# Performance work log

Measured on AMD Instinct MI355X. Metric: run time of the kernel, lower is better.

## Reference

```python
import jax, jax.numpy as jnp
import numpy as np

BETA = 0.25
GAMMA = 0.9
EPS = 1e-05
B, H, W, D, K = 64, 32, 32, 256, 1024


def setup_inputs() -> dict:
    key = jax.random.key(0)
    k1, k2 = jax.random.split(key)
    return {
        "inputs": jax.random.normal(k1, (B, H, W, D), dtype=jnp.float32),
        "codebook": jax.random.normal(k2, (D, K), dtype=jnp.float32),
        "ema_hidden_cluster": jnp.zeros((K,), dtype=jnp.float32),
        "ema_hidden_dw": jnp.zeros((D, K), dtype=jnp.float32),
        "counter": 1,  # counter after increment (fresh state: 0 + 1)
    }


def reference(inputs, codebook, ema_hidden_cluster, ema_hidden_dw, counter):
    d, k = codebook.shape
    flat = inputs.reshape(-1, d)  # [N, D]
    distances = (
        jnp.sum(jnp.square(flat), 1, keepdims=True)
        - 2.0 * jnp.matmul(flat, codebook)
        + jnp.sum(jnp.square(codebook), 0, keepdims=True)
    )
    encoding_indices = jnp.argmin(distances, axis=1)  # [N]
    encodings = jax.nn.one_hot(encoding_indices, k, dtype=distances.dtype)  # [N, K]
    flat_quantized = jnp.take(codebook, encoding_indices, axis=1).swapaxes(1, 0)  # [N, D]
    quantized = flat_quantized.reshape(inputs.shape)
    loss = BETA * jnp.mean(jnp.square(jax.lax.stop_gradient(quantized) - inputs))

    # --- EMA codebook update (training=True path) ---
    decay = jnp.float32(GAMMA)
    one = jnp.float32(1.0)
    bias = one - jnp.power(decay, counter)
    cluster_size = jnp.sum(encodings, axis=0)  # [K]
    hid_cs = ema_hidden_cluster * decay + cluster_size * (one - decay)
    avg_cs = hid_cs / bias
    dw = jnp.matmul(flat.T, encodings)  # [D, K]
    hid_dw = ema_hidden_dw * decay + dw * (one - decay)
    avg_dw = hid_dw / bias
    n = jnp.sum(avg_cs)
    smoothed_cs = (avg_cs + EPS) / (n + k * EPS) * n
    new_codebook = avg_dw / smoothed_cs[None, :]

    ste = inputs + jax.lax.stop_gradient(quantized - inputs)
    avg_probs = jnp.mean(encodings, 0)
    perplexity = jnp.exp(-jnp.sum(avg_probs * jnp.log(avg_probs + 1e-10)))
    return (ste, perplexity, loss, new_codebook)
```

## Files before the change

### kernel.cpp

```cpp
#include <hip/hip_runtime.h>

#define N 65536
#define D 256
#define K 1024
#define BETA 0.25f
#define GAMMA 0.9f
#define EPS 1e-5f

#define DWROWS 64

#define OFF_INDICES 0
#define OFF_PERM    262144
#define OFF_COUNTS  524288
#define OFF_CNORM   528384
#define OFF_OFFSETS 532480
#define OFF_CURSOR  536576
#define OFF_SMOOTH  540672
#define OFF_LOSSP   544768
#define OFF_CBT     546816
#define OFF_CBE     1595392

typedef __bf16 bf16x8 __attribute__((ext_vector_type(8)));
typedef short  s16x8  __attribute__((ext_vector_type(8)));
typedef float  f32x4  __attribute__((ext_vector_type(4)));

__device__ inline unsigned short f32_to_bf16_rn(float f) {
    unsigned int u = __float_as_uint(f);
    unsigned int r = u + 0x7fffu + ((u >> 16) & 1u);
    return (unsigned short)(r >> 16);
}

__device__ inline f32x4 mfma16(s16x8 a, s16x8 b, f32x4 c) {
    return __builtin_amdgcn_mfma_f32_16x16x32_bf16(
        __builtin_bit_cast(bf16x8, a), __builtin_bit_cast(bf16x8, b), c, 0, 0, 0);
}

__device__ __forceinline__ void stage16(const s16x8* __restrict__ g, s16x8* l) {
    __builtin_amdgcn_global_load_lds(
        (const __attribute__((address_space(1))) void*)g,
        (__attribute__((address_space(3))) void*)l, 16, 0, 0);
}

__global__ __launch_bounds__(256) void pack_cb(const float* __restrict__ cb,
                                               float* __restrict__ cbT,
                                               s16x8* __restrict__ cbEp,
                                               float* __restrict__ cnorm) {
    const int ct = blockIdx.x >> 3;
    const int c2 = (blockIdx.x >> 1) & 3;
    const int half = blockIdx.x & 1;
    const int u = half * 256 + threadIdx.x;
    const int frgc = u >> 7;
    const int ks = (u >> 6) & 1;
    const int L = u & 63;
    const int c = ct * 64 + frgc * 16 + (L & 15);
    const int d0 = c2 * 64 + (ks * 4 + (L >> 4)) * 8;
    float v[8];
    s16x8 hv, lv;
    float ss = 0.f;
#pragma unroll
    for (int j = 0; j < 8; ++j) {
        float f = cb[(size_t)(d0 + j) * K + c];
        v[j] = f;
        unsigned short h = f32_to_bf16_rn(f);
        hv[j] = (short)h;
        lv[j] = (short)f32_to_bf16_rn(f - __uint_as_float((unsigned)h << 16));
        ss = fmaf(f, f, ss);
    }
    *(float4*)&cbT[(size_t)c * D + d0]     = make_float4(v[0], v[1], v[2], v[3]);
    *(float4*)&cbT[(size_t)c * D + d0 + 4] = make_float4(v[4], v[5], v[6], v[7]);
    cbEp[(size_t)(ct * 8 + c2) * 512 + u]     = hv;
    cbEp[(size_t)(ct * 8 + 4 + c2) * 512 + u] = lv;
    atomicAdd(&cnorm[c], ss);
}

__global__ __launch_bounds__(256, 2) void argmin_mfma_kernel(
        const float* __restrict__ x,
        const s16x8* __restrict__ cbEp,
        const float* __restrict__ cnorm,
        int* __restrict__ indices) {
    __shared__ s16x8 Bs[2][1024];

    const int tid = threadIdx.x;
    const int lane = tid & 63;
    const int w = tid >> 6;
    const int r0 = blockIdx.x * 128;
    const int row16 = lane & 15;
    const int quad = lane >> 4;

#pragma unroll
    for (int i = 0; i < 4; ++i)
        stage16(cbEp + i * 256 + tid, &Bs[0][i * 256 + w * 64]);

    s16x8 Ah[2][8], Al[2][8];
#pragma unroll
    for (int frg = 0; frg < 2; ++frg) {
#pragma unroll
        for (int kb8 = 0; kb8 < 8; ++kb8) {
            const float* src = &x[(size_t)(r0 + w * 32 + frg * 16 + row16) * D
                                  + kb8 * 32 + quad * 8];
            float4 v0 = *(const float4*)src;
            float4 v1 = *(const float4*)(src + 4);
            float f[8] = {v0.x, v0.y, v0.z, v0.w, v1.x, v1.y, v1.z, v1.w};
            s16x8 hv, lv;
#pragma unroll
            for (int j = 0; j < 8; ++j) {
                unsigned short h = f32_to_bf16_rn(f[j]);
                hv[j] = (short)h;
                lv[j] = (short)f32_to_bf16_rn(f[j] - __uint_as_float((unsigned)h << 16));
            }
            Ah[frg][kb8] = hv;
            Al[frg][kb8] = lv;
        }
    }

    float minv[2][4];
    int   mini[2][4];
#pragma unroll
    for (int frg = 0; frg < 2; ++frg)
#pragma unroll
        for (int reg = 0; reg < 4; ++reg) { minv[frg][reg] = 3.4e38f; mini[frg][reg] = 0; }

    for (int ct = 0; ct < 16; ++ct) {
        f32x4 acc[2][4];
#pragma unroll
        for (int frg = 0; frg < 2; ++frg)
#pragma unroll
            for (int fc = 0; fc < 4; ++fc) acc[frg][fc] = (f32x4){0.f, 0.f, 0.f, 0.f};

#pragma unroll
        for (int ph = 0; ph < 4; ++ph) {
            __syncthreads();
            const bool has_next = !(ct == 15 && ph == 3);
            if (has_next) {
                const int nct = (ph == 3) ? ct + 1 : ct;
                const int nph = (ph == 3) ? 0 : ph + 1;
                const size_t gb = (size_t)(nct * 8 + nph * 2) * 512;
#pragma unroll
                for (int i = 0; i < 4; ++i)
                    stage16(cbEp + gb + i * 256 + tid, &Bs[(ph + 1) & 1][i * 256 + w * 64]);
            }
#pragma unroll
            for (int half = 0; half < 2; ++half) {
                const int cchunk = ph * 2 + half;
                const int c2 = cchunk & 3;
#pragma unroll
                for (int ks = 0; ks < 2; ++ks) {
                    const int ksb = c2 * 2 + ks;
#pragma unroll
                    for (int fc = 0; fc < 4; ++fc) {
                        s16x8 b = Bs[ph & 1][half * 512 + (fc * 2 + ks) * 64 + lane];
#pragma unroll
                        for (int frg = 0; frg < 2; ++frg) {
                            acc[frg][fc] = mfma16(Ah[frg][ksb], b, acc[frg][fc]);
                            if (cchunk < 4)
                                acc[frg][fc] = mfma16(Al[frg][ksb], b, acc[frg][fc]);
                        }
                    }
                }
            }
        }
#pragma unroll
        for (int fc = 0; fc < 4; ++fc) {
            int col = ct * 64 + fc * 16 + row16;
            float cn = cnorm[col];
#pragma unroll
            for (int frg = 0; frg < 2; ++frg)
#pragma unroll
                for (int reg = 0; reg < 4; ++reg) {
                    float val = fmaf(-2.f, acc[frg][fc][reg], cn);
                    if (val < minv[frg][reg]) { minv[frg][reg] = val; mini[frg][reg] = col; }
                }
        }
    }

#pragma unroll
    for (int mask = 1; mask <= 8; mask <<= 1) {
#pragma unroll
        for (int frg = 0; frg < 2; ++frg)
#pragma unroll
            for (int reg = 0; reg < 4; ++reg) {
                float ov = __shfl_xor(minv[frg][reg], mask, 64);
                int   oi = __shfl_xor(mini[frg][reg], mask, 64);
                if (ov < minv[frg][reg] ||
                    (ov == minv[frg][reg] && oi < mini[frg][reg])) {
                    minv[frg][reg] = ov; mini[frg][reg] = oi;
                }
            }
    }
    if (row16 == 0) {
#pragma unroll
        for (int frg = 0; frg < 2; ++frg)
#pragma unroll
            for (int reg = 0; reg < 4; ++reg)
                indices[r0 + w * 32 + frg * 16 + quad * 4 + reg] = mini[frg][reg];
    }
}

__global__ __launch_bounds__(1024) void finalize_kernel(const int* __restrict__ indices,
                                                        const float* __restrict__ ema_c,
                                                        const int* __restrict__ counter,
                                                        float* __restrict__ out_perp,
                                                        int* __restrict__ cursor,
                                                        float* __restrict__ smoothed) {
    const int k = threadIdx.x;
    const int lane = k & 63;
    const int wave = k >> 6;
    __shared__ int hist[1024];
    __shared__ float wsum[16], went[16];
    __shared__ int wtot[16];

    hist[k] = 0;
    __syncthreads();
    const int4* idx4 = (const int4*)indices;
#pragma unroll 4
    for (int i = 0; i < 16; ++i) {
        int4 v = idx4[(size_t)i * 1024 + k];
        atomicAdd(&hist[v.x], 1);
        atomicAdd(&hist[v.y], 1);
        atomicAdd(&hist[v.z], 1);
        atomicAdd(&hist[v.w], 1);
    }
    __syncthreads();

    const int c = hist[k];
    const float bias = 1.0f - powf(GAMMA, (float)counter[0]);
    const float avg = fmaf(ema_c[k], GAMMA, (float)c * (1.0f - GAMMA)) / bias;
    const float p = (float)c * (1.0f / (float)N);
    const float ent = p * logf(p + 1e-10f);

    float a = avg, e = ent;
#pragma unroll
    for (int off = 32; off >= 1; off >>= 1) {
        a += __shfl_down(a, off, 64);
        e += __shfl_down(e, off, 64);
    }
    int v = c;
#pragma unroll
    for (int off = 1; off < 64; off <<= 1) {
        int t = __shfl_up(v, off, 64);
        if (lane >= off) v += t;
    }
    if (lane == 0)  { wsum[wave] = a; went[wave] = e; }
    if (lane == 63) { wtot[wave] = v; }
    __syncthreads();

    float nsum = 0.f, entt = 0.f;
    int woff = 0;
#pragma unroll
    for (int i = 0; i < 16; ++i) {
        nsum += wsum[i];
        entt += went[i];
        if (i < wave) woff += wtot[i];
    }
    cursor[k] = woff + v - c;
    smoothed[k] = (avg + EPS) / (nsum + (float)K * EPS) * nsum;
    if (k == 0) out_perp[0] = expf(-entt);
}

__global__ __launch_bounds__(256) void scatter_kernel(const int* __restrict__ indices,
                                                      int* __restrict__ cursor,
                                                      int* __restrict__ permk,
                                                      float* __restrict__ dwT) {
    const int n = blockIdx.x * 256 + threadIdx.x;
    *(float4*)&dwT[(size_t)n * 4] = make_float4(0.f, 0.f, 0.f, 0.f);
    const int k = indices[n];
    const int pos = atomicAdd(&cursor[k], 1);
    permk[pos] = n | (k << 16);
}

__global__ __launch_bounds__(256) void dw_fused_kernel(const float* __restrict__ x,
                                                       const float* __restrict__ cbT,
                                                       const int* __restrict__ permk,
                                                       float* __restrict__ ste,
                                                       float* __restrict__ dwT,
                                                       float* __restrict__ lossp) {
    __shared__ int s_rows[DWROWS];
    __shared__ int s_keys[DWROWS];
    const int tid = threadIdx.x;
    const int g = tid >> 6;
    const int d4 = tid & 63;
    const int base = blockIdx.x * DWROWS;
    if (tid < DWROWS) {
        const int pk = permk[base + tid];
        s_rows[tid] = pk & 0xffff;
        s_keys[tid] = pk >> 16;
    }
    __syncthreads();

    const float4* x4   = (const float4*)x;
    const float4* cbT4 = (const float4*)cbT;
    float4*       ste4 = (float4*)ste;

    float ax = 0.f, ay = 0.f, az = 0.f, aw = 0.f;
    float ls = 0.f;
    const int r0 = g * 16;
#pragma unroll
    for (int i = 0; i < 16; ++i) {
        const int r = r0 + i;
        const int n = s_rows[r];
        const int k = s_keys[r];
        const float4 xv = x4[(size_t)n * 64 + d4];
        const float4 q  = cbT4[(size_t)k * 64 + d4];
        ste4[(size_t)n * 64 + d4] = q;
        ax += xv.x; ay += xv.y; az += xv.z; aw += xv.w;
        float dx = q.x - xv.x, dy = q.y - xv.y, dz = q.z - xv.z, dw = q.w - xv.w;
        ls = fmaf(dx, dx, ls); ls = fmaf(dy, dy, ls);
        ls = fmaf(dz, dz, ls); ls = fmaf(dw, dw, ls);
        const int nk = (i == 15) ? -1 : s_keys[r + 1];
        if (nk != k) {
            float* dst = &dwT[(size_t)k * D + d4 * 4];
            atomicAdd(dst + 0, ax);
            atomicAdd(dst + 1, ay);
            atomicAdd(dst + 2, az);
            atomicAdd(dst + 3, aw);
            ax = ay = az = aw = 0.f;
        }
    }
#pragma unroll
    for (int off = 32; off >= 1; off >>= 1) ls += __shfl_down(ls, off, 64);
    __shared__ float red[4];
    if ((tid & 63) == 0) red[tid >> 6] = ls;
    __syncthreads();
    if (tid == 0) lossp[blockIdx.x] = red[0] + red[1] + red[2] + red[3];
}

__global__ __launch_bounds__(256) void codebook_final_kernel(const float* __restrict__ dwT,
                                                             const float* __restrict__ ema_dw,
                                                             const float* __restrict__ smoothed,
                                                             const int* __restrict__ counter,
                                                             const float* __restrict__ lossp,
                                                             float* __restrict__ out_cb,
                                                             float* __restrict__ out_loss) {
    __shared__ float tile[64][65];
    __shared__ float lred[4];
    const int tid = threadIdx.x;

    if (blockIdx.x == 0) {
        float s = lossp[tid] + lossp[tid + 256] + lossp[tid + 512] + lossp[tid + 768];
#pragma unroll
        for (int off = 32; off >= 1; off >>= 1) s += __shfl_down(s, off, 64);
        if ((tid & 63) == 0) lred[tid >> 6] = s;
        __syncthreads();
        if (tid == 0)
            out_loss[0] = BETA * (lred[0] + lred[1] + lred[2] + lred[3])
                          * (1.0f / ((float)N * (float)D));
        __syncthreads();
    }

    const int d0 = (blockIdx.x & 3) * 64;
    const int k0 = (blockIdx.x >> 2) * 64;
#pragma unroll
    for (int it = 0; it < 16; ++it) {
        int idx = it * 256 + tid;
        int kk = idx >> 6, dd = idx & 63;
        tile[kk][dd] = dwT[(size_t)(k0 + kk) * D + d0 + dd];
    }
    __syncthreads();
    const float bias = 1.0f - powf(GAMMA, (float)counter[0]);
#pragma unroll
    for (int it = 0; it < 16; ++it) {
        int idx = it * 256 + tid;
        int dd = idx >> 6, kk = idx & 63;
        float dwv = tile[kk][dd];
        float hid = fmaf(ema_dw[(size_t)(d0 + dd) * K + k0 + kk], GAMMA,
                         dwv * (1.0f - GAMMA));
        out_cb[(size_t)(d0 + dd) * K + k0 + kk] = (hid / bias) / smoothed[k0 + kk];
    }
}

extern "C" void kernel_launch(void* const* d_in, const int* in_sizes, int n_in,
                              void* d_out, int out_size, void* d_ws, size_t ws_size,
                              hipStream_t stream) {
    const float* x       = (const float*)d_in[0];
    const float* cb      = (const float*)d_in[1];
    const float* ema_c   = (const float*)d_in[2];
    const float* ema_dw  = (const float*)d_in[3];
    const int*   counter = (const int*)d_in[4];

    float* out = (float*)d_out;
    float* ste = out;
    float* out_perp = out + (size_t)N * D;
    float* out_loss = out_perp + 1;
    float* out_cb = out_perp + 2;

    char* ws = (char*)d_ws;
    int* indices  = (int*)(ws + OFF_INDICES);
    int* permk    = (int*)(ws + OFF_PERM);
    float* cnorm  = (float*)(ws + OFF_CNORM);
    int* cursor   = (int*)(ws + OFF_CURSOR);
    float* smooth = (float*)(ws + OFF_SMOOTH);
    float* cbT    = (float*)(ws + OFF_CBT);
    s16x8* cbEp   = (s16x8*)(ws + OFF_CBE);
    float* dwT    = (float*)(ws + OFF_CBE);
    float* lossp  = (float*)(ws + OFF_CNORM);

    hipMemsetAsync(cnorm, 0, K * sizeof(float), stream);

    pack_cb<<<128, 256, 0, stream>>>(cb, cbT, cbEp, cnorm);
    argmin_mfma_kernel<<<N / 128, 256, 0, stream>>>(x, cbEp, cnorm, indices);
    finalize_kernel<<<1, 1024, 0, stream>>>(indices, ema_c, counter,
                                            out_perp, cursor, smooth);
    scatter_kernel<<<N / 256, 256, 0, stream>>>(indices, cursor, permk, dwT);
    dw_fused_kernel<<<N / DWROWS, 256, 0, stream>>>(x, cbT, permk, ste, dwT, lossp);
    codebook_final_kernel<<<64, 256, 0, stream>>>(dwT, ema_dw, smooth, counter,
                                                  lossp, out_cb, out_loss);
}
```

Baseline: 308.6 us.

## Fuse scatter into single-block finalize and remove atomics from codebook packing

Codebook packing now assigns each wave a full column strip so norms are reduced with shuffles and stored directly, removing the memset and global atomics. The separate scatter kernel is folded into the single-block finalize kernel, which keeps indices in registers, uses an LDS cursor, and also zeroes the dw accumulator. This saves launches and global cursor atomics but serializes the scatter and 1 MB zeroing onto a single workgroup.

```diff
diff --git a/kernel.cpp b/kernel.cpp
--- a/kernel.cpp
+++ b/kernel.cpp
@@ -45,32 +45,37 @@
                                                float* __restrict__ cbT,
                                                s16x8* __restrict__ cbEp,
                                                float* __restrict__ cnorm) {
-    const int ct = blockIdx.x >> 3;
-    const int c2 = (blockIdx.x >> 1) & 3;
-    const int half = blockIdx.x & 1;
-    const int u = half * 256 + threadIdx.x;
-    const int frgc = u >> 7;
-    const int ks = (u >> 6) & 1;
-    const int L = u & 63;
-    const int c = ct * 64 + frgc * 16 + (L & 15);
-    const int d0 = c2 * 64 + (ks * 4 + (L >> 4)) * 8;
-    float v[8];
-    s16x8 hv, lv;
+    const int ct = blockIdx.x;
+    const int w  = threadIdx.x >> 6;
+    const int L  = threadIdx.x & 63;
+    const int c  = ct * 64 + w * 16 + (L & 15);
     float ss = 0.f;
 #pragma unroll
-    for (int j = 0; j < 8; ++j) {
-        float f = cb[(size_t)(d0 + j) * K + c];
-        v[j] = f;
-        unsigned short h = f32_to_bf16_rn(f);
-        hv[j] = (short)h;
-        lv[j] = (short)f32_to_bf16_rn(f - __uint_as_float((unsigned)h << 16));
-        ss = fmaf(f, f, ss);
-    }
-    *(float4*)&cbT[(size_t)c * D + d0]     = make_float4(v[0], v[1], v[2], v[3]);
-    *(float4*)&cbT[(size_t)c * D + d0 + 4] = make_float4(v[4], v[5], v[6], v[7]);
-    cbEp[(size_t)(ct * 8 + c2) * 512 + u]     = hv;
-    cbEp[(size_t)(ct * 8 + 4 + c2) * 512 + u] = lv;
-    atomicAdd(&cnorm[c], ss);
+    for (int c2 = 0; c2 < 4; ++c2) {
+#pragma unroll
+        for (int ks = 0; ks < 2; ++ks) {
+            const int d0 = c2 * 64 + (ks * 4 + (L >> 4)) * 8;
+            const int u  = w * 128 + ks * 64 + L;
+            float v[8];
+            s16x8 hv, lv;
+#pragma unroll
+            for (int j = 0; j < 8; ++j) {
+                float f = cb[(size_t)(d0 + j) * K + c];
+                v[j] = f;
+                unsigned short h = f32_to_bf16_rn(f);
+                hv[j] = (short)h;
+                lv[j] = (short)f32_to_bf16_rn(f - __uint_as_float((unsigned)h << 16));
+                ss = fmaf(f, f, ss);
+            }
+            *(float4*)&cbT[(size_t)c * D + d0]     = make_float4(v[0], v[1], v[2], v[3]);
+            *(float4*)&cbT[(size_t)c * D + d0 + 4] = make_float4(v[4], v[5], v[6], v[7]);
+            cbEp[(size_t)(ct * 8 + c2) * 512 + u]     = hv;
+            cbEp[(size_t)(ct * 8 + 4 + c2) * 512 + u] = lv;
+        }
+    }
+    ss += __shfl_xor(ss, 16, 64);
+    ss += __shfl_xor(ss, 32, 64);
+    if ((L >> 4) == 0) cnorm[c] = ss;
 }
 
 __global__ __launch_bounds__(256, 2) void argmin_mfma_kernel(
@@ -196,29 +201,38 @@
     }
 }
 
-__global__ __launch_bounds__(1024) void finalize_kernel(const int* __restrict__ indices,
-                                                        const float* __restrict__ ema_c,
-                                                        const int* __restrict__ counter,
-                                                        float* __restrict__ out_perp,
-                                                        int* __restrict__ cursor,
-                                                        float* __restrict__ smoothed) {
+__global__ __launch_bounds__(1024) void finalize_scatter_kernel(
+        const int* __restrict__ indices,
+        const float* __restrict__ ema_c,
+        const int* __restrict__ counter,
+        float* __restrict__ out_perp,
+        float* __restrict__ smoothed,
+        int* __restrict__ permk,
+        float* __restrict__ dwT) {
     const int k = threadIdx.x;
     const int lane = k & 63;
     const int wave = k >> 6;
     __shared__ int hist[1024];
+    __shared__ int curs[1024];
     __shared__ float wsum[16], went[16];
     __shared__ int wtot[16];
 
     hist[k] = 0;
-    __syncthreads();
+    float4* dwT4 = (float4*)dwT;
+    const float4 z = make_float4(0.f, 0.f, 0.f, 0.f);
+#pragma unroll 8
+    for (int i = 0; i < 64; ++i) dwT4[(size_t)i * 1024 + k] = z;
+    __syncthreads();
+
     const int4* idx4 = (const int4*)indices;
-#pragma unroll 4
+    int4 v[16];
+#pragma unroll
     for (int i = 0; i < 16; ++i) {
-        int4 v = idx4[(size_t)i * 1024 + k];
-        atomicAdd(&hist[v.x], 1);
-        atomicAdd(&hist[v.y], 1);
-        atomicAdd(&hist[v.z], 1);
-        atomicAdd(&hist[v.w], 1);
+        v[i] = idx4[(size_t)i * 1024 + k];
+        atomicAdd(&hist[v[i].x], 1);
+        atomicAdd(&hist[v[i].y], 1);
+        atomicAdd(&hist[v[i].z], 1);
+        atomicAdd(&hist[v[i].w], 1);
     }
     __syncthreads();
 
@@ -234,14 +248,14 @@
         a += __shfl_down(a, off, 64);
         e += __shfl_down(e, off, 64);
     }
-    int v = c;
+    int sv = c;
 #pragma unroll
     for (int off = 1; off < 64; off <<= 1) {
-        int t = __shfl_up(v, off, 64);
-        if (lane >= off) v += t;
+        int t = __shfl_up(sv, off, 64);
+        if (lane >= off) sv += t;
     }
     if (lane == 0)  { wsum[wave] = a; went[wave] = e; }
-    if (lane == 63) { wtot[wave] = v; }
+    if (lane == 63) { wtot[wave] = sv; }
     __syncthreads();
 
     float nsum = 0.f, entt = 0.f;
@@ -252,20 +266,20 @@
         entt += went[i];
         if (i < wave) woff += wtot[i];
     }
-    cursor[k] = woff + v - c;
+    curs[k] = woff + sv - c;
     smoothed[k] = (avg + EPS) / (nsum + (float)K * EPS) * nsum;
     if (k == 0) out_perp[0] = expf(-entt);
-}
-
-__global__ __launch_bounds__(256) void scatter_kernel(const int* __restrict__ indices,
-                                                      int* __restrict__ cursor,
-                                                      int* __restrict__ permk,
-                                                      float* __restrict__ dwT) {
-    const int n = blockIdx.x * 256 + threadIdx.x;
-    *(float4*)&dwT[(size_t)n * 4] = make_float4(0.f, 0.f, 0.f, 0.f);
-    const int k = indices[n];
-    const int pos = atomicAdd(&cursor[k], 1);
-    permk[pos] = n | (k << 16);
+    __syncthreads();
+
+#pragma unroll
+    for (int i = 0; i < 16; ++i) {
+        const int n0 = (i * 1024 + k) * 4;
+        int pos;
+        pos = atomicAdd(&curs[v[i].x], 1); permk[pos] = (n0 + 0) | (v[i].x << 16);
+        pos = atomicAdd(&curs[v[i].y], 1); permk[pos] = (n0 + 1) | (v[i].y << 16);
+        pos = atomicAdd(&curs[v[i].z], 1); permk[pos] = (n0 + 2) | (v[i].z << 16);
+        pos = atomicAdd(&curs[v[i].w], 1); permk[pos] = (n0 + 3) | (v[i].w << 16);
+    }
 }
 
 __global__ __launch_bounds__(256) void dw_fused_kernel(const float* __restrict__ x,
@@ -387,20 +401,16 @@
     int* indices  = (int*)(ws + OFF_INDICES);
     int* permk    = (int*)(ws + OFF_PERM);
     float* cnorm  = (float*)(ws + OFF_CNORM);
-    int* cursor   = (int*)(ws + OFF_CURSOR);
     float* smooth = (float*)(ws + OFF_SMOOTH);
     float* cbT    = (float*)(ws + OFF_CBT);
     s16x8* cbEp   = (s16x8*)(ws + OFF_CBE);
     float* dwT    = (float*)(ws + OFF_CBE);
     float* lossp  = (float*)(ws + OFF_CNORM);
 
-    hipMemsetAsync(cnorm, 0, K * sizeof(float), stream);
-
-    pack_cb<<<128, 256, 0, stream>>>(cb, cbT, cbEp, cnorm);
+    pack_cb<<<16, 256, 0, stream>>>(cb, cbT, cbEp, cnorm);
     argmin_mfma_kernel<<<N / 128, 256, 0, stream>>>(x, cbEp, cnorm, indices);
-    finalize_kernel<<<1, 1024, 0, stream>>>(indices, ema_c, counter,
-                                            out_perp, cursor, smooth);
-    scatter_kernel<<<N / 256, 256, 0, stream>>>(indices, cursor, permk, dwT);
+    finalize_scatter_kernel<<<1, 1024, 0, stream>>>(indices, ema_c, counter,
+                                                    out_perp, smooth, permk, dwT);
     dw_fused_kernel<<<N / DWROWS, 256, 0, stream>>>(x, cbT, permk, ste, dwT, lossp);
     codebook_final_kernel<<<64, 256, 0, stream>>>(dwT, ema_dw, smooth, counter,
                                                   lossp, out_cb, out_loss);
```

After: 311.9 us. No clear change (+1.1%).
